# Kernel tuning notes

Hardware: AMD Instinct MI355X
Metric: run time of the kernel (lower is better)

## Reference

```python
import jax, jax.numpy as jnp
import numpy as np

B, N, A, H, MID = 256, 128, 15, 32, 256  # batch, nodes(=in_channels), actions, EQL-proxy hidden, critic mid_weight


def _glorot(k, shape):
    lim = float(np.sqrt(6.0 / (shape[0] + shape[1])))
    return jax.random.uniform(k, shape, jnp.float32, -lim, lim)


def setup_inputs() -> dict:
    key = jax.random.key(0)
    ks = jax.random.split(key, 10)
    obs = jax.random.normal(ks[0], (B, N), jnp.float32)
    return dict(
        obs=obs,
        # messenger EQL proxy: 4 -> H -> 1
        mw1=_glorot(ks[1], (4, H)), mb1=jnp.zeros((H,), jnp.float32),
        mw2=_glorot(ks[2], (H, 1)), mb2=jnp.zeros((1,), jnp.float32),
        # actor EQL proxy: 3 -> H -> 1
        aw1=_glorot(ks[3], (3, H)), ab1=jnp.zeros((H,), jnp.float32),
        aw2=_glorot(ks[4], (H, 1)), ab2=jnp.zeros((1,), jnp.float32),
        # critic MLP: N -> MID -> MID -> MID -> 1 (depth=4)
        cw1=_glorot(ks[5], (N, MID)), cb1=jnp.zeros((MID,), jnp.float32),
        cw2=_glorot(ks[6], (MID, MID)), cb2=jnp.zeros((MID,), jnp.float32),
        cw3=_glorot(ks[7], (MID, MID)), cb3=jnp.zeros((MID,), jnp.float32),
        cw4=_glorot(ks[8], (MID, 1)), cb4=jnp.zeros((1,), jnp.float32),
    )


def reference(obs, mw1, mb1, mw2, mb2, aw1, ab1, aw2, ab2,
              cw1, cb1, cw2, cb2, cw3, cb3, cw4, cb4):
    b, n = obs.shape
    coor = jnp.arange(n, dtype=jnp.float32) / n  # append_index coordinate channel
    x = jnp.stack([obs, jnp.broadcast_to(coor, obs.shape)], axis=-1)  # [B,n,2]

    # all-pairs message pass: msg_in[b,i,j] = concat(x[b,i], x[b,j])  -> [B,n,n,4]
    xi = jnp.broadcast_to(x[:, :, None, :], (b, n, n, 2))
    xj = jnp.broadcast_to(x[:, None, :, :], (b, n, n, 2))
    msg_in = jnp.concatenate([xi, xj], axis=-1)
    messages = jax.nn.relu(msg_in @ mw1 + mb1) @ mw2 + mb2  # [B,n,n,1]
    msg = jnp.sum(messages, axis=-2)[..., 0]  # sum over j, squeeze -> [B,n]

    # append_index again on the aggregated messages
    m = jnp.stack([msg, jnp.broadcast_to(coor, msg.shape)], axis=-1)  # [B,n,2]

    # node x action cross: am[b,i,a] = concat(m[b,i], a)  -> [B,n,A,3]
    acts = jnp.arange(A, dtype=jnp.float32)[None, None, :, None]
    mi = jnp.broadcast_to(m[:, :, None, :], (b, n, A, 2))
    aj = jnp.broadcast_to(acts, (b, n, A, 1))
    am = jnp.concatenate([mi, aj], axis=-1)
    am_messages = jax.nn.relu(am @ aw1 + ab1) @ aw2 + ab2  # [B,n,A,1]
    logits = jnp.sum(am_messages, axis=-3)[..., 0]  # sum over nodes (obs_dim=-3) -> [B,A]

    # critic MLP on raw obs
    h = jax.nn.relu(obs @ cw1 + cb1)
    h = jax.nn.relu(h @ cw2 + cb2)
    h = jax.nn.relu(h @ cw3 + cb3)
    value = h @ cw4 + cb4  # [B,1]
    return logits, value
```

## Files before the change

kernel.cpp:

```cpp
#include <hip/hip_runtime.h>

#define BB   256
#define NN   128
#define AA   15
#define HH   32
#define MIDD 256

__global__ __launch_bounds__(512, 4) void gacq_v4(
    const float* __restrict__ obs,
    const float* __restrict__ mw1, const float* __restrict__ mb1,
    const float* __restrict__ mw2, const float* __restrict__ mb2,
    const float* __restrict__ aw1, const float* __restrict__ ab1,
    const float* __restrict__ aw2, const float* __restrict__ ab2,
    const float* __restrict__ cw1, const float* __restrict__ cb1,
    const float* __restrict__ cw2, const float* __restrict__ cb2,
    const float* __restrict__ cw3, const float* __restrict__ cb3,
    const float* __restrict__ cw4, const float* __restrict__ cb4,
    float* __restrict__ out)
{
    __shared__ __align__(16) float aux_s[356];
    __shared__ __align__(16) float obs_s[NN];
    __shared__ __align__(16) float vp_s[NN][HH];
    __shared__ __align__(16) float part_s[4][8][16][8];
    __shared__ __align__(16) float msg_s[NN];
    __shared__ __align__(16) float cpart_s[8][MIDD];
    __shared__ __align__(16) float h_s[2][MIDD];
    __shared__ float red_s[4];

    const int blk = blockIdx.x;
    const int t   = threadIdx.x;

    if (blk < BB) {
        const int b = blk;

        if (t < 354) {
            float v;
            if      (t < 128) v = mw1[t];
            else if (t < 224) v = aw1[t - 128];
            else if (t < 256) v = ab1[t - 224];
            else if (t < 288) v = aw2[t - 256];
            else if (t < 320) v = mw2[t - 288];
            else if (t < 352) v = mb1[t - 320];
            else if (t == 352) v = mb2[0];
            else               v = ab2[0];
            aux_s[t] = v;
        }
        if (t < NN) obs_s[t] = obs[b * NN + t];
        __syncthreads();

        for (int e = t; e < NN * HH; e += 512) {
            const int j = e >> 5, k = e & 31;
            vp_s[j][k] = obs_s[j] * aux_s[64 + k]
                       + ((float)j * (1.0f / (float)NN)) * aux_s[96 + k]
                       + aux_s[320 + k];
        }

        const int kg = t & 7;
        const int rg = (t >> 3) & 15;
        const int jg = t >> 7;

        float u[8][4];
        const float w20 = aux_s[288 + kg * 4 + 0];
        const float w21 = aux_s[288 + kg * 4 + 1];
        const float w22 = aux_s[288 + kg * 4 + 2];
        const float w23 = aux_s[288 + kg * 4 + 3];
#pragma unroll
        for (int rr = 0; rr < 8; ++rr) {
            const int   row = rg * 8 + rr;
            const float ob  = obs_s[row];
            const float cr  = (float)row * (1.0f / (float)NN);
#pragma unroll
            for (int kk = 0; kk < 4; ++kk)
                u[rr][kk] = ob * aux_s[kg * 4 + kk] + cr * aux_s[32 + kg * 4 + kk];
        }
        __syncthreads();

        float acc[8];
#pragma unroll
        for (int rr = 0; rr < 8; ++rr) acc[rr] = 0.f;
        const int    j0    = jg * 32;
        const float* vbase = &vp_s[0][kg * 4];
        float4 vc = *(const float4*)(vbase + j0 * HH);
#pragma unroll 4
        for (int jj = 0; jj < 32; ++jj) {
            const int    nj = j0 + ((jj + 1) & 31);
            const float4 vn = *(const float4*)(vbase + nj * HH);
#pragma unroll
            for (int rr = 0; rr < 8; ++rr) {
                acc[rr] += fmaxf(u[rr][0] + vc.x, 0.f) * w20;
                acc[rr] += fmaxf(u[rr][1] + vc.y, 0.f) * w21;
                acc[rr] += fmaxf(u[rr][2] + vc.z, 0.f) * w22;
                acc[rr] += fmaxf(u[rr][3] + vc.w, 0.f) * w23;
            }
            vc = vn;
        }
        *(float4*)&part_s[jg][kg][rg][0] = make_float4(acc[0], acc[1], acc[2], acc[3]);
        *(float4*)&part_s[jg][kg][rg][4] = make_float4(acc[4], acc[5], acc[6], acc[7]);
        __syncthreads();

        if (t < NN) {
            float m = (float)NN * aux_s[352];
#pragma unroll
            for (int g = 0; g < 4; ++g)
#pragma unroll
                for (int q = 0; q < 8; ++q)
                    m += part_s[g][q][t >> 3][t & 7];
            msg_s[t] = m;
        }
        __syncthreads();

#pragma unroll
        for (int it = 0; it < 2; ++it) {
            const int   row = t & 127;
            const int   c   = (t >> 7) + it * 4;
            const float mi  = msg_s[row];
            const float cr  = (float)row * (1.0f / (float)NN);
            const int   k0  = c * 4;
            float4 p;
            p.x = mi * aux_s[128 + k0 + 0] + cr * aux_s[160 + k0 + 0] + aux_s[224 + k0 + 0];
            p.y = mi * aux_s[128 + k0 + 1] + cr * aux_s[160 + k0 + 1] + aux_s[224 + k0 + 1];
            p.z = mi * aux_s[128 + k0 + 2] + cr * aux_s[160 + k0 + 2] + aux_s[224 + k0 + 2];
            p.w = mi * aux_s[128 + k0 + 3] + cr * aux_s[160 + k0 + 3] + aux_s[224 + k0 + 3];
            *(float4*)&vp_s[row][(c ^ (row & 7)) * 4] = p;
        }
        __syncthreads();

        {
            const int   a   = t >> 5;
            const int   sub = t & 31;
            const float fa  = (float)a;
            float qa[HH];
#pragma unroll
            for (int k = 0; k < HH; ++k) qa[k] = fa * aux_s[192 + k];
            float s0 = 0.f, s1 = 0.f, s2 = 0.f, s3 = 0.f;
#pragma unroll
            for (int m = 0; m < 4; ++m) {
                const int row = sub + 32 * m;
                const int sw  = row & 7;
#pragma unroll
                for (int c = 0; c < 8; ++c) {
                    const float4 p4 = *(const float4*)&vp_s[row][(c ^ sw) * 4];
                    const float4 w4 = *(const float4*)&aux_s[256 + c * 4];
                    const int    k0 = c * 4;
                    s0 += fmaxf(p4.x + qa[k0 + 0], 0.f) * w4.x;
                    s1 += fmaxf(p4.y + qa[k0 + 1], 0.f) * w4.y;
                    s2 += fmaxf(p4.z + qa[k0 + 2], 0.f) * w4.z;
                    s3 += fmaxf(p4.w + qa[k0 + 3], 0.f) * w4.w;
                }
            }
            float s = (s0 + s1) + (s2 + s3);
#pragma unroll
            for (int off = 1; off < 32; off <<= 1) s += __shfl_xor(s, off);
            if (sub == 0 && a < AA)
                out[b * AA + a] = s + (float)NN * aux_s[353];
        }
    } else {
        const int b = blk - BB;
        if (t < NN) obs_s[t] = obs[b * NN + t];
        __syncthreads();

        const int q = t & 63;
        const int s = t >> 6;

        {
            float4 acc = make_float4(0.f, 0.f, 0.f, 0.f);
            const int k0 = s * 16;
#pragma unroll 4
            for (int k = k0; k < k0 + 16; ++k) {
                const float4 w = *(const float4*)&cw1[k * MIDD + q * 4];
                const float  h = obs_s[k];
                acc.x += h * w.x; acc.y += h * w.y; acc.z += h * w.z; acc.w += h * w.w;
            }
            *(float4*)&cpart_s[s][q * 4] = acc;
        }
        __syncthreads();
        if (t < MIDD) {
            float sum = cb1[t];
#pragma unroll
            for (int s8 = 0; s8 < 8; ++s8) sum += cpart_s[s8][t];
            h_s[0][t] = fmaxf(sum, 0.f);
        }
        __syncthreads();

        {
            float4 acc = make_float4(0.f, 0.f, 0.f, 0.f);
            const int k0 = s * 32;
#pragma unroll 4
            for (int k = k0; k < k0 + 32; ++k) {
                const float4 w = *(const float4*)&cw2[k * MIDD + q * 4];
                const float  h = h_s[0][k];
                acc.x += h * w.x; acc.y += h * w.y; acc.z += h * w.z; acc.w += h * w.w;
            }
            *(float4*)&cpart_s[s][q * 4] = acc;
        }
        __syncthreads();
        if (t < MIDD) {
            float sum = cb2[t];
#pragma unroll
            for (int s8 = 0; s8 < 8; ++s8) sum += cpart_s[s8][t];
            h_s[1][t] = fmaxf(sum, 0.f);
        }
        __syncthreads();

        {
            float4 acc = make_float4(0.f, 0.f, 0.f, 0.f);
            const int k0 = s * 32;
#pragma unroll 4
            for (int k = k0; k < k0 + 32; ++k) {
                const float4 w = *(const float4*)&cw3[k * MIDD + q * 4];
                const float  h = h_s[1][k];
                acc.x += h * w.x; acc.y += h * w.y; acc.z += h * w.z; acc.w += h * w.w;
            }
            *(float4*)&cpart_s[s][q * 4] = acc;
        }
        __syncthreads();
        if (t < MIDD) {
            float sum = cb3[t];
#pragma unroll
            for (int s8 = 0; s8 < 8; ++s8) sum += cpart_s[s8][t];
            const float h3 = fmaxf(sum, 0.f);
            float pv = h3 * cw4[t];
#pragma unroll
            for (int off = 32; off > 0; off >>= 1) pv += __shfl_xor(pv, off);
            if ((t & 63) == 0) red_s[t >> 6] = pv;
        }
        __syncthreads();
        if (t == 0)
            out[BB * AA + b] = red_s[0] + red_s[1] + red_s[2] + red_s[3] + cb4[0];
    }
}

extern "C" void kernel_launch(void* const* d_in, const int* in_sizes, int n_in,
                              void* d_out, int out_size, void* d_ws, size_t ws_size,
                              hipStream_t stream) {
    const float* obs = (const float*)d_in[0];
    const float* mw1 = (const float*)d_in[1];
    const float* mb1 = (const float*)d_in[2];
    const float* mw2 = (const float*)d_in[3];
    const float* mb2 = (const float*)d_in[4];
    const float* aw1 = (const float*)d_in[5];
    const float* ab1 = (const float*)d_in[6];
    const float* aw2 = (const float*)d_in[7];
    const float* ab2 = (const float*)d_in[8];
    const float* cw1 = (const float*)d_in[9];
    const float* cb1 = (const float*)d_in[10];
    const float* cw2 = (const float*)d_in[11];
    const float* cb2 = (const float*)d_in[12];
    const float* cw3 = (const float*)d_in[13];
    const float* cb3 = (const float*)d_in[14];
    const float* cw4 = (const float*)d_in[15];
    const float* cb4 = (const float*)d_in[16];
    float* out = (float*)d_out;

    gacq_v4<<<dim3(2 * BB), dim3(512), 0, stream>>>(
        obs, mw1, mb1, mw2, mb2, aw1, ab1, aw2, ab2,
        cw1, cb1, cw2, cb2, cw3, cb3, cw4, cb4, out);
}
```

Baseline: 19.69 us.

## Use packed fp16 dot2 for message pass and batch four rows per critic block

The all-pairs message inner loop now stores the per-node projections in fp16 and uses packed half adds, packed max and fdot2 with fp32 accumulation, which halves LDS traffic and the ALU op count. The critic branch processes four batch rows per block, two per thread, so each weight load is reused, and the grid shrinks from 512 to 320 blocks. Shared memory is overlaid through a union to cut LDS footprint. Rounding the message-MLP hidden values to fp16 risks accuracy loss.

New measurement: 26.12 us. 32.6% more time.

```diff
diff --git a/kernel.cpp b/kernel.cpp
--- a/kernel.cpp
+++ b/kernel.cpp
@@ -6,7 +6,21 @@
 #define HH   32
 #define MIDD 256
 
-__global__ __launch_bounds__(512, 4) void gacq_v4(
+typedef _Float16 h2_t __attribute__((ext_vector_type(2)));
+
+struct MsgS {
+    _Float16 vh[NN][HH];
+    float    p[NN][HH];
+    float    part[4][8][16][8];
+    float    msg[NN];
+};
+struct CriS {
+    float obs4[4][NN];
+    float cpart[4][4][MIDD];
+    float h4[2][4][MIDD];
+};
+
+__global__ __launch_bounds__(512, 4) void gacq_v7(
     const float* __restrict__ obs,
     const float* __restrict__ mw1, const float* __restrict__ mb1,
     const float* __restrict__ mw2, const float* __restrict__ mb2,
@@ -20,12 +34,7 @@
 {
     __shared__ __align__(16) float aux_s[356];
     __shared__ __align__(16) float obs_s[NN];
-    __shared__ __align__(16) float vp_s[NN][HH];
-    __shared__ __align__(16) float part_s[4][8][16][8];
-    __shared__ __align__(16) float msg_s[NN];
-    __shared__ __align__(16) float cpart_s[8][MIDD];
-    __shared__ __align__(16) float h_s[2][MIDD];
-    __shared__ float red_s[4];
+    __shared__ __align__(16) union { MsgS m; CriS c; } u_s;
 
     const int blk = blockIdx.x;
     const int t   = threadIdx.x;
@@ -48,54 +57,69 @@
         if (t < NN) obs_s[t] = obs[b * NN + t];
         __syncthreads();
 
-        for (int e = t; e < NN * HH; e += 512) {
-            const int j = e >> 5, k = e & 31;
-            vp_s[j][k] = obs_s[j] * aux_s[64 + k]
-                       + ((float)j * (1.0f / (float)NN)) * aux_s[96 + k]
-                       + aux_s[320 + k];
+        for (int e = t; e < NN * HH / 2; e += 512) {
+            const int   j  = e >> 4, kp = e & 15;
+            const int   k0 = kp * 2;
+            const float cj = (float)j * (1.0f / (float)NN);
+            const float v0 = obs_s[j] * aux_s[64 + k0]     + cj * aux_s[96 + k0]     + aux_s[320 + k0];
+            const float v1 = obs_s[j] * aux_s[64 + k0 + 1] + cj * aux_s[96 + k0 + 1] + aux_s[320 + k0 + 1];
+            h2_t p; p[0] = (_Float16)v0; p[1] = (_Float16)v1;
+            *(h2_t*)&u_s.m.vh[j][k0] = p;
         }
 
         const int kg = t & 7;
         const int rg = (t >> 3) & 15;
         const int jg = t >> 7;
 
-        float u[8][4];
-        const float w20 = aux_s[288 + kg * 4 + 0];
-        const float w21 = aux_s[288 + kg * 4 + 1];
-        const float w22 = aux_s[288 + kg * 4 + 2];
-        const float w23 = aux_s[288 + kg * 4 + 3];
+        h2_t u2[8][2], w2h[2];
+        {
+            w2h[0][0] = (_Float16)aux_s[288 + kg * 4 + 0];
+            w2h[0][1] = (_Float16)aux_s[288 + kg * 4 + 1];
+            w2h[1][0] = (_Float16)aux_s[288 + kg * 4 + 2];
+            w2h[1][1] = (_Float16)aux_s[288 + kg * 4 + 3];
+        }
 #pragma unroll
         for (int rr = 0; rr < 8; ++rr) {
             const int   row = rg * 8 + rr;
             const float ob  = obs_s[row];
             const float cr  = (float)row * (1.0f / (float)NN);
 #pragma unroll
-            for (int kk = 0; kk < 4; ++kk)
-                u[rr][kk] = ob * aux_s[kg * 4 + kk] + cr * aux_s[32 + kg * 4 + kk];
+            for (int kp = 0; kp < 2; ++kp) {
+                const int k0 = kg * 4 + kp * 2;
+                u2[rr][kp][0] = (_Float16)(ob * aux_s[k0]     + cr * aux_s[32 + k0]);
+                u2[rr][kp][1] = (_Float16)(ob * aux_s[k0 + 1] + cr * aux_s[32 + k0 + 1]);
+            }
         }
         __syncthreads();
 
         float acc[8];
 #pragma unroll
         for (int rr = 0; rr < 8; ++rr) acc[rr] = 0.f;
-        const int    j0    = jg * 32;
-        const float* vbase = &vp_s[0][kg * 4];
-        float4 vc = *(const float4*)(vbase + j0 * HH);
+        const int j0 = jg * 32;
+        {
+            const h2_t   zero  = (h2_t)((_Float16)0);
+            const uint2* vbase = (const uint2*)&u_s.m.vh[0][kg * 4];
+            uint2 vc = vbase[j0 * 8];
 #pragma unroll 4
-        for (int jj = 0; jj < 32; ++jj) {
-            const int    nj = j0 + ((jj + 1) & 31);
-            const float4 vn = *(const float4*)(vbase + nj * HH);
-#pragma unroll
-            for (int rr = 0; rr < 8; ++rr) {
-                acc[rr] += fmaxf(u[rr][0] + vc.x, 0.f) * w20;
-                acc[rr] += fmaxf(u[rr][1] + vc.y, 0.f) * w21;
-                acc[rr] += fmaxf(u[rr][2] + vc.z, 0.f) * w22;
-                acc[rr] += fmaxf(u[rr][3] + vc.w, 0.f) * w23;
-            }
-            vc = vn;
-        }
-        *(float4*)&part_s[jg][kg][rg][0] = make_float4(acc[0], acc[1], acc[2], acc[3]);
-        *(float4*)&part_s[jg][kg][rg][4] = make_float4(acc[4], acc[5], acc[6], acc[7]);
+            for (int jj = 0; jj < 32; ++jj) {
+                const int   nj = j0 + ((jj + 1) & 31);
+                const uint2 vn = vbase[nj * 8];
+                const h2_t  va = __builtin_bit_cast(h2_t, vc.x);
+                const h2_t  vb = __builtin_bit_cast(h2_t, vc.y);
+#pragma unroll
+                for (int rr = 0; rr < 8; ++rr) {
+                    h2_t s0 = u2[rr][0] + va;
+                    h2_t s1 = u2[rr][1] + vb;
+                    s0 = __builtin_elementwise_max(s0, zero);
+                    s1 = __builtin_elementwise_max(s1, zero);
+                    acc[rr] = __builtin_amdgcn_fdot2(s0, w2h[0], acc[rr], false);
+                    acc[rr] = __builtin_amdgcn_fdot2(s1, w2h[1], acc[rr], false);
+                }
+                vc = vn;
+            }
+        }
+        *(float4*)&u_s.m.part[jg][kg][rg][0] = make_float4(acc[0], acc[1], acc[2], acc[3]);
+        *(float4*)&u_s.m.part[jg][kg][rg][4] = make_float4(acc[4], acc[5], acc[6], acc[7]);
         __syncthreads();
 
         if (t < NN) {
@@ -104,8 +128,8 @@
             for (int g = 0; g < 4; ++g)
 #pragma unroll
                 for (int q = 0; q < 8; ++q)
-                    m += part_s[g][q][t >> 3][t & 7];
-            msg_s[t] = m;
+                    m += u_s.m.part[g][q][t >> 3][t & 7];
+            u_s.m.msg[t] = m;
         }
         __syncthreads();
 
@@ -113,7 +137,7 @@
         for (int it = 0; it < 2; ++it) {
             const int   row = t & 127;
             const int   c   = (t >> 7) + it * 4;
-            const float mi  = msg_s[row];
+            const float mi  = u_s.m.msg[row];
             const float cr  = (float)row * (1.0f / (float)NN);
             const int   k0  = c * 4;
             float4 p;
@@ -121,7 +145,7 @@
             p.y = mi * aux_s[128 + k0 + 1] + cr * aux_s[160 + k0 + 1] + aux_s[224 + k0 + 1];
             p.z = mi * aux_s[128 + k0 + 2] + cr * aux_s[160 + k0 + 2] + aux_s[224 + k0 + 2];
             p.w = mi * aux_s[128 + k0 + 3] + cr * aux_s[160 + k0 + 3] + aux_s[224 + k0 + 3];
-            *(float4*)&vp_s[row][(c ^ (row & 7)) * 4] = p;
+            *(float4*)&u_s.m.p[row][(c ^ (row & 7)) * 4] = p;
         }
         __syncthreads();
 
@@ -139,7 +163,7 @@
                 const int sw  = row & 7;
 #pragma unroll
                 for (int c = 0; c < 8; ++c) {
-                    const float4 p4 = *(const float4*)&vp_s[row][(c ^ sw) * 4];
+                    const float4 p4 = *(const float4*)&u_s.m.p[row][(c ^ sw) * 4];
                     const float4 w4 = *(const float4*)&aux_s[256 + c * 4];
                     const int    k0 = c * 4;
                     s0 += fmaxf(p4.x + qa[k0 + 0], 0.f) * w4.x;
@@ -155,78 +179,102 @@
                 out[b * AA + a] = s + (float)NN * aux_s[353];
         }
     } else {
-        const int b = blk - BB;
-        if (t < NN) obs_s[t] = obs[b * NN + t];
-        __syncthreads();
-
-        const int q = t & 63;
-        const int s = t >> 6;
-
-        {
-            float4 acc = make_float4(0.f, 0.f, 0.f, 0.f);
-            const int k0 = s * 16;
-#pragma unroll 4
-            for (int k = k0; k < k0 + 16; ++k) {
-                const float4 w = *(const float4*)&cw1[k * MIDD + q * 4];
-                const float  h = obs_s[k];
-                acc.x += h * w.x; acc.y += h * w.y; acc.z += h * w.z; acc.w += h * w.w;
-            }
-            *(float4*)&cpart_s[s][q * 4] = acc;
-        }
-        __syncthreads();
-        if (t < MIDD) {
-            float sum = cb1[t];
-#pragma unroll
-            for (int s8 = 0; s8 < 8; ++s8) sum += cpart_s[s8][t];
-            h_s[0][t] = fmaxf(sum, 0.f);
-        }
-        __syncthreads();
-
-        {
-            float4 acc = make_float4(0.f, 0.f, 0.f, 0.f);
+        const int b0 = (blk - BB) * 4;
+
+        for (int e = t; e < 4 * NN; e += 512)
+            u_s.c.obs4[e >> 7][e & 127] = obs[(b0 + (e >> 7)) * NN + (e & 127)];
+        __syncthreads();
+
+        const int q  = t & 63;
+        const int pp = (t >> 6) & 1;
+        const int s  = t >> 7;
+        const int ba = pp * 2, bb2 = pp * 2 + 1;
+
+        {
+            float4 A0 = make_float4(0.f, 0.f, 0.f, 0.f);
+            float4 A1 = make_float4(0.f, 0.f, 0.f, 0.f);
             const int k0 = s * 32;
-#pragma unroll 4
+#pragma unroll 8
             for (int k = k0; k < k0 + 32; ++k) {
-                const float4 w = *(const float4*)&cw2[k * MIDD + q * 4];
-                const float  h = h_s[0][k];
-                acc.x += h * w.x; acc.y += h * w.y; acc.z += h * w.z; acc.w += h * w.w;
-            }
-            *(float4*)&cpart_s[s][q * 4] = acc;
-        }
-        __syncthreads();
-        if (t < MIDD) {
-            float sum = cb2[t];
-#pragma unroll
-            for (int s8 = 0; s8 < 8; ++s8) sum += cpart_s[s8][t];
-            h_s[1][t] = fmaxf(sum, 0.f);
-        }
-        __syncthreads();
-
-        {
-            float4 acc = make_float4(0.f, 0.f, 0.f, 0.f);
-            const int k0 = s * 32;
-#pragma unroll 4
-            for (int k = k0; k < k0 + 32; ++k) {
-                const float4 w = *(const float4*)&cw3[k * MIDD + q * 4];
-                const float  h = h_s[1][k];
-                acc.x += h * w.x; acc.y += h * w.y; acc.z += h * w.z; acc.w += h * w.w;
-            }
-            *(float4*)&cpart_s[s][q * 4] = acc;
-        }
-        __syncthreads();
-        if (t < MIDD) {
-            float sum = cb3[t];
-#pragma unroll
-            for (int s8 = 0; s8 < 8; ++s8) sum += cpart_s[s8][t];
-            const float h3 = fmaxf(sum, 0.f);
-            float pv = h3 * cw4[t];
-#pragma unroll
-            for (int off = 32; off > 0; off >>= 1) pv += __shfl_xor(pv, off);
-            if ((t & 63) == 0) red_s[t >> 6] = pv;
-        }
-        __syncthreads();
-        if (t == 0)
-            out[BB * AA + b] = red_s[0] + red_s[1] + red_s[2] + red_s[3] + cb4[0];
+                const float4 w  = *(const float4*)&cw1[k * MIDD + q * 4];
+                const float  h0 = u_s.c.obs4[ba][k];
+                const float  h1 = u_s.c.obs4[bb2][k];
+                A0.x += h0 * w.x; A0.y += h0 * w.y; A0.z += h0 * w.z; A0.w += h0 * w.w;
+                A1.x += h1 * w.x; A1.y += h1 * w.y; A1.z += h1 * w.z; A1.w += h1 * w.w;
+            }
+            *(float4*)&u_s.c.cpart[s][ba][q * 4]  = A0;
+            *(float4*)&u_s.c.cpart[s][bb2][q * 4] = A1;
+        }
+        __syncthreads();
+        for (int e = t; e < 4 * MIDD; e += 512) {
+            const int bb = e >> 8, o = e & 255;
+            float sum = cb1[o];
+#pragma unroll
+            for (int ss = 0; ss < 4; ++ss) sum += u_s.c.cpart[ss][bb][o];
+            u_s.c.h4[0][bb][o] = fmaxf(sum, 0.f);
+        }
+        __syncthreads();
+
+        {
+            float4 A0 = make_float4(0.f, 0.f, 0.f, 0.f);
+            float4 A1 = make_float4(0.f, 0.f, 0.f, 0.f);
+            const int k0 = s * 64;
+#pragma unroll 8
+            for (int k = k0; k < k0 + 64; ++k) {
+                const float4 w  = *(const float4*)&cw2[k * MIDD + q * 4];
+                const float  h0 = u_s.c.h4[0][ba][k];
+                const float  h1 = u_s.c.h4[0][bb2][k];
+                A0.x += h0 * w.x; A0.y += h0 * w.y; A0.z += h0 * w.z; A0.w += h0 * w.w;
+                A1.x += h1 * w.x; A1.y += h1 * w.y; A1.z += h1 * w.z; A1.w += h1 * w.w;
+            }
+            *(float4*)&u_s.c.cpart[s][ba][q * 4]  = A0;
+            *(float4*)&u_s.c.cpart[s][bb2][q * 4] = A1;
+        }
+        __syncthreads();
+        for (int e = t; e < 4 * MIDD; e += 512) {
+            const int bb = e >> 8, o = e & 255;
+            float sum = cb2[o];
+#pragma unroll
+            for (int ss = 0; ss < 4; ++ss) sum += u_s.c.cpart[ss][bb][o];
+            u_s.c.h4[1][bb][o] = fmaxf(sum, 0.f);
+        }
+        __syncthreads();
+
+        {
+            float4 A0 = make_float4(0.f, 0.f, 0.f, 0.f);
+            float4 A1 = make_float4(0.f, 0.f, 0.f, 0.f);
+            const int k0 = s * 64;
+#pragma unroll 8
+            for (int k = k0; k < k0 + 64; ++k) {
+                const float4 w  = *(const float4*)&cw3[k * MIDD + q * 4];
+                const float  h0 = u_s.c.h4[1][ba][k];
+                const float  h1 = u_s.c.h4[1][bb2][k];
+                A0.x += h0 * w.x; A0.y += h0 * w.y; A0.z += h0 * w.z; A0.w += h0 * w.w;
+                A1.x += h1 * w.x; A1.y += h1 * w.y; A1.z += h1 * w.z; A1.w += h1 * w.w;
+            }
+            *(float4*)&u_s.c.cpart[s][ba][q * 4]  = A0;
+            *(float4*)&u_s.c.cpart[s][bb2][q * 4] = A1;
+        }
+        __syncthreads();
+        for (int e = t; e < 4 * MIDD; e += 512) {
+            const int bb = e >> 8, o = e & 255;
+            float sum = cb3[o];
+#pragma unroll
+            for (int ss = 0; ss < 4; ++ss) sum += u_s.c.cpart[ss][bb][o];
+            u_s.c.h4[0][bb][o] = fmaxf(sum, 0.f) * cw4[o];
+        }
+        __syncthreads();
+        {
+            const int wv   = t >> 6;
+            const int lane = t & 63;
+            if (wv < 4) {
+                float sum = u_s.c.h4[0][wv][lane]       + u_s.c.h4[0][wv][lane + 64]
+                          + u_s.c.h4[0][wv][lane + 128] + u_s.c.h4[0][wv][lane + 192];
+#pragma unroll
+                for (int off = 32; off > 0; off >>= 1) sum += __shfl_xor(sum, off);
+                if (lane == 0) out[BB * AA + b0 + wv] = sum + cb4[0];
+            }
+        }
     }
 }
 
@@ -252,7 +300,7 @@
     const float* cb4 = (const float*)d_in[16];
     float* out = (float*)d_out;
 
-    gacq_v4<<<dim3(2 * BB), dim3(512), 0, stream>>>(
+    gacq_v7<<<dim3(BB + BB / 4), dim3(512), 0, stream>>>(
         obs, mw1, mb1, mw2, mb2, aw1, ab1, aw2, ab2,
         cw1, cb1, cw2, cb2, cw3, cb3, cw4, cb4, out);
 }
```
